# Kernel optimization log

Hardware: AMD Instinct MI355X
Metric: run time of the kernel (lower is better)

The kernel has to match this reference:

```python
import jax, jax.numpy as jnp
import numpy as np

N_HEAD, D_HEAD, D_MODEL, MAX_LEN = 16, 64, 1024, 64
T, B = 1024, 4
SCALE = 1.0 / D_HEAD ** 0.5


def setup_inputs() -> dict:
    key = jax.random.key(0)
    k1, k2, k3, k4 = jax.random.split(key, 4)
    s = 0.02
    w = jax.random.normal(k1, (T, B, D_MODEL), jnp.float32)
    Wqkv = jax.random.normal(k2, (3 * N_HEAD * D_HEAD, D_MODEL), jnp.float32) * s
    pos_emb = jax.random.normal(k3, (2 * MAX_LEN + 1, D_HEAD), jnp.float32) * s
    Wo = jax.random.normal(k4, (D_MODEL, N_HEAD * D_HEAD), jnp.float32) * s
    i = jnp.arange(T)
    # causal mask, 3D path of the original: [qlen, klen, bsz], True = masked
    attn_mask = jnp.broadcast_to((i[None, :] > i[:, None])[:, :, None], (T, T, B))
    return {"w": w, "attn_mask": attn_mask, "Wqkv": Wqkv, "pos_emb": pos_emb, "Wo": Wo}


def reference(w, attn_mask, Wqkv, pos_emb, Wo):
    qlen, bsz, _ = w.shape
    klen = qlen
    # qkv projection (no bias), chunk into q, k, v
    heads = jnp.einsum('tbd,ed->tbe', w, Wqkv)            # [T, B, 3*H*Dh]
    q, k, v = jnp.split(heads, 3, axis=-1)
    q = q.reshape(qlen, bsz, N_HEAD, D_HEAD).transpose(1, 2, 0, 3) * SCALE  # [B,H,T,Dh]
    k = k.reshape(klen, bsz, N_HEAD, D_HEAD).transpose(1, 2, 0, 3)
    v = v.reshape(klen, bsz, N_HEAD, D_HEAD).transpose(1, 2, 0, 3)
    # learnable relative position embeddings r[q_pos, k_pos, Dh]
    i = jnp.arange(klen)
    rel = jnp.clip(i[None, :] - i[:, None], -MAX_LEN, MAX_LEN) + MAX_LEN   # [T, T]
    r = pos_emb[rel]                                                       # [T, T, Dh]
    # content score + relative-position score (q already scaled)
    qk = jnp.einsum('bhqd,bhkd->bhqk', q, k)
    qr = jnp.einsum('bhqd,qkd->bhqk', q, r)
    score = qk + qr                                                        # [B,H,T,T]
    m = attn_mask.transpose(2, 0, 1)[:, None]                              # [B,1,T,T]
    score = jnp.where(m, -jnp.inf, score)
    attn = jax.nn.softmax(score, axis=-1)                                  # coverage
    # content context + position context
    ctx = jnp.einsum('bhqk,bhkd->bhqd', attn, v) + jnp.einsum('bhqk,qkd->bhqd', attn, r)
    attn_vec = ctx.transpose(0, 2, 1, 3).reshape(bsz, qlen, N_HEAD * D_HEAD)
    out = jnp.einsum('bte,de->btd', attn_vec, Wo)                          # [B,T,D]
    return jnp.swapaxes(out, 0, 1)                                         # [T,B,D]
```

## Files before the change

kernel.cpp:

```cpp
#include <hip/hip_runtime.h>
#include <hip/hip_bf16.h>
#include <math.h>

#define N_HEAD 16
#define D_HEAD 64
#define T_SEQ 1024
#define BATCH 4
#define QSCALE 0.180336879f

typedef float f32x4 __attribute__((ext_vector_type(4)));
typedef short bf16x8 __attribute__((ext_vector_type(8)));
typedef short bf16x4v __attribute__((ext_vector_type(4)));

#define AS1(p) ((const __attribute__((address_space(1))) void*)(p))
#define AS3(p) ((__attribute__((address_space(3))) void*)(p))

__device__ inline bf16x8 ld8(const __hip_bfloat16* p) {
    bf16x4v lo = *(const bf16x4v*)p;
    bf16x4v hi = *(const bf16x4v*)(p + 4);
    return __builtin_shufflevector(lo, hi, 0, 1, 2, 3, 4, 5, 6, 7);
}

__global__ __launch_bounds__(256) void cast_all(
    const float* __restrict__ s0, __hip_bfloat16* __restrict__ d0, int n0,
    const float* __restrict__ s1, __hip_bfloat16* __restrict__ d1, int n1) {
    int i = (blockIdx.x * 256 + threadIdx.x) * 8;
    const float* src;
    __hip_bfloat16* dst;
    if (i < n0) { src = s0 + i; dst = d0 + i; }
    else if ((i -= n0) < n1) { src = s1 + i; dst = d1 + i; }
    else return;
    float4 a = *(const float4*)src;
    float4 b = *(const float4*)(src + 4);
    __hip_bfloat16 t[8];
    t[0] = __float2bfloat16(a.x); t[1] = __float2bfloat16(a.y);
    t[2] = __float2bfloat16(a.z); t[3] = __float2bfloat16(a.w);
    t[4] = __float2bfloat16(b.x); t[5] = __float2bfloat16(b.y);
    t[6] = __float2bfloat16(b.z); t[7] = __float2bfloat16(b.w);
    *(uint4*)dst = *(const uint4*)t;
}

__global__ __launch_bounds__(256) void qkv_gemm_mfma(
    const __hip_bfloat16* __restrict__ A,
    const __hip_bfloat16* __restrict__ B,
    const float* __restrict__ P,
    __hip_bfloat16* __restrict__ Qb, __hip_bfloat16* __restrict__ Kb,
    __hip_bfloat16* __restrict__ Vtb) {
    constexpr int Kd = 1024;
    __shared__ __hip_bfloat16 As[128 * 32];
    __shared__ __hip_bfloat16 Bs[128 * 32];
    const int tid = threadIdx.x;
    const int w = tid >> 6, lane = tid & 63;
    const int lanelo = lane & 15, quad = lane >> 4;
    const int wm = (w >> 1) * 64, wn = (w & 1) * 64;
    const int m0 = blockIdx.y * 128, n0 = blockIdx.x * 128;

    const __hip_bfloat16* Ag = A + (size_t)(m0 + w * 16 + (lane >> 2)) * Kd + (lane & 3) * 8;
    const __hip_bfloat16* Bg = B + (size_t)(n0 + w * 16 + (lane >> 2)) * Kd + (lane & 3) * 8;
    __hip_bfloat16* AsW0 = As + w * 16 * 32;
    __hip_bfloat16* AsW1 = As + (64 + w * 16) * 32;
    __hip_bfloat16* BsW0 = Bs + w * 16 * 32;
    __hip_bfloat16* BsW1 = Bs + (64 + w * 16) * 32;

    f32x4 acc[4][4];
#pragma unroll
    for (int i = 0; i < 4; i++)
#pragma unroll
        for (int j = 0; j < 4; j++) acc[i][j] = (f32x4){0.f, 0.f, 0.f, 0.f};

    for (int k0 = 0; k0 < Kd; k0 += 32) {
        __syncthreads();
        __builtin_amdgcn_global_load_lds(AS1(Ag + k0), AS3(AsW0), 16, 0, 0);
        __builtin_amdgcn_global_load_lds(AS1(Ag + 64 * Kd + k0), AS3(AsW1), 16, 0, 0);
        __builtin_amdgcn_global_load_lds(AS1(Bg + k0), AS3(BsW0), 16, 0, 0);
        __builtin_amdgcn_global_load_lds(AS1(Bg + 64 * Kd + k0), AS3(BsW1), 16, 0, 0);
        __syncthreads();
        bf16x8 af[4], bfr[4];
#pragma unroll
        for (int i = 0; i < 4; i++)
            af[i] = *(const bf16x8*)(As + (wm + i * 16 + lanelo) * 32 + quad * 8);
#pragma unroll
        for (int j = 0; j < 4; j++)
            bfr[j] = *(const bf16x8*)(Bs + (wn + j * 16 + lanelo) * 32 + quad * 8);
#pragma unroll
        for (int i = 0; i < 4; i++)
#pragma unroll
            for (int j = 0; j < 4; j++)
                acc[i][j] = __builtin_amdgcn_mfma_f32_16x16x32_bf16(af[i], bfr[j], acc[i][j], 0, 0, 0);
    }

    const int part = n0 >> 10;
    float p0v[4] = {0.f, 0.f, 0.f, 0.f};
    if (part == 2) {
#pragma unroll
        for (int j = 0; j < 4; j++) p0v[j] = P[j * 16 + lanelo];
    }
#pragma unroll
    for (int i = 0; i < 4; i++)
#pragma unroll
        for (int j = 0; j < 4; j++)
#pragma unroll
            for (int reg = 0; reg < 4; reg++) {
                const int row = m0 + wm + i * 16 + quad * 4 + reg;
                const int col = n0 + wn + j * 16 + lanelo;
                const int t = row >> 2, b = row & 3;
                const int e = col & 1023, h = e >> 6, d = e & 63;
                const float v = acc[i][j][reg];
                if (part == 0)
                    Qb[((size_t)(b * 16 + h) * 1024 + t) * 64 + d] = __float2bfloat16(v * QSCALE);
                else if (part == 1)
                    Kb[((size_t)(b * 16 + h) * 1024 + t) * 64 + d] = __float2bfloat16(v);
                else
                    Vtb[((size_t)(b * 16 + h) * 64 + d) * 1024 + t] = __float2bfloat16(v + p0v[j]);
            }
}

__global__ __launch_bounds__(256) void out_gemm_mfma(
    const __hip_bfloat16* __restrict__ A,
    const __hip_bfloat16* __restrict__ B,
    float* __restrict__ out) {
    constexpr int Kd = 1024;
    __shared__ __hip_bfloat16 As[128 * 64];
    __shared__ __hip_bfloat16 Bs[64 * 64];
    const int tid = threadIdx.x;
    const int w = tid >> 6, lane = tid & 63;
    const int lanelo = lane & 15, quad = lane >> 4;
    const int wm = (w >> 1) * 64, wn = (w & 1) * 32;
    const int m0 = blockIdx.y * 128, n0 = blockIdx.x * 64;

    const int sr = lane >> 3;
    const int sc = ((lane & 7) ^ sr) * 8;
    const __hip_bfloat16* Ag = A + (size_t)(m0 + w * 32 + sr) * Kd + sc;
    const __hip_bfloat16* Bg = B + (size_t)(n0 + w * 16 + sr) * Kd + sc;
    __hip_bfloat16* AsW = As + w * 2048;
    __hip_bfloat16* BsW = Bs + w * 1024;

    f32x4 acc[4][2];
#pragma unroll
    for (int i = 0; i < 4; i++)
#pragma unroll
        for (int j = 0; j < 2; j++) acc[i][j] = (f32x4){0.f, 0.f, 0.f, 0.f};

    const int cswz = lanelo & 7;

    for (int k0 = 0; k0 < Kd; k0 += 64) {
        __syncthreads();
#pragma unroll
        for (int i = 0; i < 4; i++)
            __builtin_amdgcn_global_load_lds(AS1(Ag + k0 + i * 8 * Kd), AS3(AsW + i * 512), 16, 0, 0);
#pragma unroll
        for (int i = 0; i < 2; i++)
            __builtin_amdgcn_global_load_lds(AS1(Bg + k0 + i * 8 * Kd), AS3(BsW + i * 512), 16, 0, 0);
        __syncthreads();
#pragma unroll
        for (int h = 0; h < 2; h++) {
            const int c16 = (((h * 4 + quad) ^ cswz)) * 8;
            bf16x8 af[4], bfr[2];
#pragma unroll
            for (int i = 0; i < 4; i++)
                af[i] = *(const bf16x8*)(As + (size_t)(wm + i * 16 + lanelo) * 64 + c16);
#pragma unroll
            for (int j = 0; j < 2; j++)
                bfr[j] = *(const bf16x8*)(Bs + (size_t)(wn + j * 16 + lanelo) * 64 + c16);
#pragma unroll
            for (int i = 0; i < 4; i++)
#pragma unroll
                for (int j = 0; j < 2; j++)
                    acc[i][j] = __builtin_amdgcn_mfma_f32_16x16x32_bf16(af[i], bfr[j], acc[i][j], 0, 0, 0);
        }
    }

#pragma unroll
    for (int i = 0; i < 4; i++)
#pragma unroll
        for (int j = 0; j < 2; j++)
#pragma unroll
            for (int reg = 0; reg < 4; reg++) {
                const int row = m0 + wm + i * 16 + quad * 4 + reg;
                const int col = n0 + wn + j * 16 + lanelo;
                const int b = row >> 10, t = row & 1023;
                out[(size_t)(t * 4 + b) * 1024 + col] = acc[i][j][reg];
            }
}

__global__ __launch_bounds__(256) void flash_attn(
    const __hip_bfloat16* __restrict__ Qb,
    const __hip_bfloat16* __restrict__ Kb,
    const __hip_bfloat16* __restrict__ Vtb,
    const float* __restrict__ P,
    const float* __restrict__ Wo,
    __hip_bfloat16* __restrict__ Wob,
    __hip_bfloat16* __restrict__ av) {
    __shared__ __hip_bfloat16 Ks[64][72];
    __shared__ __hip_bfloat16 Vs[64][72];
    __shared__ __hip_bfloat16 Pl[4][16][68];
    __shared__ __hip_bfloat16 Pband[4][2][16][68];
    __shared__ __hip_bfloat16 QPl[4][2][16][66];

    const int px = blockIdx.x;
    const int TB = 15 - px, TS = px;
    const int bh = blockIdx.y;
    const int b = bh >> 4, h = bh & 15;
    const int tid = threadIdx.x;

    {
        const int gid = (bh * 8 + px) * 256 + tid;
        const float4 a = *(const float4*)(Wo + (size_t)gid * 8);
        const float4 c = *(const float4*)(Wo + (size_t)gid * 8 + 4);
        __hip_bfloat16 t[8];
        t[0] = __float2bfloat16(a.x); t[1] = __float2bfloat16(a.y);
        t[2] = __float2bfloat16(a.z); t[3] = __float2bfloat16(a.w);
        t[4] = __float2bfloat16(c.x); t[5] = __float2bfloat16(c.y);
        t[6] = __float2bfloat16(c.z); t[7] = __float2bfloat16(c.w);
        *(uint4*)(Wob + (size_t)gid * 8) = *(const uint4*)t;
    }

    const int w = tid >> 6, lane = tid & 63;
    const int lanelo = lane & 15, quad = lane >> 4;
    const size_t qkbase = (size_t)bh * 1024 * 64;
    const size_t vbase  = (size_t)bh * 64 * 1024;

    const int sr = tid >> 2;
    const int sc = (tid & 3) << 4;
    const __hip_bfloat16* kgb = Kb + qkbase + (size_t)sr * 64 + sc;
    const __hip_bfloat16* vgb = Vtb + vbase + (size_t)sr * 1024 + sc;

    {
        short* pb = (short*)&Pband[w][0][0][0];
        for (int i = lane; i < 2 * 16 * 68; i += 64) pb[i] = 0;
    }

    bf16x8 aqb0, aqb1, aqs0, aqs1;
    {
        const __hip_bfloat16* qrb = Qb + qkbase + (size_t)(TB * 64 + w * 16 + lanelo) * 64;
        aqb0 = *(const bf16x8*)(qrb + quad * 8);
        aqb1 = *(const bf16x8*)(qrb + 32 + quad * 8);
        const __hip_bfloat16* qrs = Qb + qkbase + (size_t)(TS * 64 + w * 16 + lanelo) * 64;
        aqs0 = *(const bf16x8*)(qrs + quad * 8);
        aqs1 = *(const bf16x8*)(qrs + 32 + quad * 8);
    }

#pragma unroll
    for (int jj = 0; jj < 5; jj++) {
        const float* prow = P + (size_t)(jj * 16 + lanelo) * 64 + quad * 8;
        float4 pa = *(const float4*)prow;
        float4 pb = *(const float4*)(prow + 4);
        float4 pc = *(const float4*)(prow + 32);
        float4 pd = *(const float4*)(prow + 36);
        __hip_bfloat16 t0[8], t1[8];
        t0[0] = __float2bfloat16(pa.x); t0[1] = __float2bfloat16(pa.y);
        t0[2] = __float2bfloat16(pa.z); t0[3] = __float2bfloat16(pa.w);
        t0[4] = __float2bfloat16(pb.x); t0[5] = __float2bfloat16(pb.y);
        t0[6] = __float2bfloat16(pb.z); t0[7] = __float2bfloat16(pb.w);
        t1[0] = __float2bfloat16(pc.x); t1[1] = __float2bfloat16(pc.y);
        t1[2] = __float2bfloat16(pc.z); t1[3] = __float2bfloat16(pc.w);
        t1[4] = __float2bfloat16(pd.x); t1[5] = __float2bfloat16(pd.y);
        t1[6] = __float2bfloat16(pd.z); t1[7] = __float2bfloat16(pd.w);
        f32x4 accB = (f32x4){0.f, 0.f, 0.f, 0.f};
        accB = __builtin_amdgcn_mfma_f32_16x16x32_bf16(aqb0, *(const bf16x8*)t0, accB, 0, 0, 0);
        accB = __builtin_amdgcn_mfma_f32_16x16x32_bf16(aqb1, *(const bf16x8*)t1, accB, 0, 0, 0);
        f32x4 accS = (f32x4){0.f, 0.f, 0.f, 0.f};
        accS = __builtin_amdgcn_mfma_f32_16x16x32_bf16(aqs0, *(const bf16x8*)t0, accS, 0, 0, 0);
        accS = __builtin_amdgcn_mfma_f32_16x16x32_bf16(aqs1, *(const bf16x8*)t1, accS, 0, 0, 0);
#pragma unroll
        for (int reg = 0; reg < 4; reg++) {
            QPl[w][0][quad * 4 + reg][jj * 16 + lanelo] = __float2bfloat16(accB[reg]);
            QPl[w][1][quad * 4 + reg][jj * 16 + lanelo] = __float2bfloat16(accS[reg]);
        }
    }
    float qp0b[4], qp0s[4];
#pragma unroll
    for (int reg = 0; reg < 4; reg++) {
        qp0b[reg] = (float)QPl[w][0][quad * 4 + reg][0];
        qp0s[reg] = (float)QPl[w][1][quad * 4 + reg][0];
    }

    f32x4 o_accB[4], o_lB, o_accS[4], o_lS;
#pragma unroll
    for (int dt = 0; dt < 4; dt++) {
        o_accB[dt] = (f32x4){0.f, 0.f, 0.f, 0.f};
        o_accS[dt] = (f32x4){0.f, 0.f, 0.f, 0.f};
    }
    o_lB = (f32x4){0.f, 0.f, 0.f, 0.f};
    o_lS = (f32x4){0.f, 0.f, 0.f, 0.f};
    const short one_bf = 0x3F80;
    const bf16x8 vones = {one_bf, one_bf, one_bf, one_bf, one_bf, one_bf, one_bf, one_bf};

    auto do_qtile = [&](int tq, int Tq, const bf16x8& a0, const bf16x8& a1,
                        const float* qp0, f32x4* o_acc, f32x4& o_l, int kt) {
        f32x4 s_acc[4];
        __builtin_amdgcn_s_setprio(1);
#pragma unroll
        for (int ct = 0; ct < 4; ct++) {
            bf16x8 b0 = *(const bf16x8*)&Ks[ct * 16 + lanelo][quad * 8];
            bf16x8 b1 = *(const bf16x8*)&Ks[ct * 16 + lanelo][32 + quad * 8];
            f32x4 acc = (f32x4){0.f, 0.f, 0.f, 0.f};
            acc = __builtin_amdgcn_mfma_f32_16x16x32_bf16(a0, b0, acc, 0, 0, 0);
            acc = __builtin_amdgcn_mfma_f32_16x16x32_bf16(a1, b1, acc, 0, 0, 0);
            s_acc[ct] = acc;
        }
        __builtin_amdgcn_s_setprio(0);
        const int q0 = Tq * 64 + w * 16;
        const int obase = q0 - kt * 64;
        if (kt < Tq - 1) {
#pragma unroll
            for (int ct = 0; ct < 4; ct++)
#pragma unroll
                for (int reg = 0; reg < 4; reg++) {
                    const float p = __builtin_exp2f(s_acc[ct][reg] + qp0[reg]);
                    Pl[w][quad * 4 + reg][ct * 16 + lanelo] = __float2bfloat16(p);
                }
        } else {
#pragma unroll
            for (int ct = 0; ct < 4; ct++)
#pragma unroll
                for (int reg = 0; reg < 4; reg++) {
                    const int rloc = quad * 4 + reg;
                    const int kl = ct * 16 + lanelo;
                    const int o = obase + rloc - kl;
                    const int idx = (o >= 64 || o < 0) ? 0 : (64 - o);
                    const float add = (float)QPl[w][tq][rloc][idx];
                    const float p = (o < 0) ? 0.f : __builtin_exp2f(s_acc[ct][reg] + add);
                    const __hip_bfloat16 pbv = __float2bfloat16(p);
                    Pl[w][rloc][kl] = pbv;
                    if (o >= 0 && o <= 63) Pband[w][tq][rloc][63 - o] = pbv;
                }
        }
        __builtin_amdgcn_s_setprio(1);
#pragma unroll
        for (int c = 0; c < 2; c++) {
            bf16x8 ap = ld8(&Pl[w][lanelo][c * 32 + quad * 8]);
#pragma unroll
            for (int dt = 0; dt < 4; dt++) {
                bf16x8 bv = *(const bf16x8*)&Vs[dt * 16 + lanelo][c * 32 + quad * 8];
                o_acc[dt] = __builtin_amdgcn_mfma_f32_16x16x32_bf16(ap, bv, o_acc[dt], 0, 0, 0);
            }
            o_l = __builtin_amdgcn_mfma_f32_16x16x32_bf16(ap, vones, o_l, 0, 0, 0);
        }
        __builtin_amdgcn_s_setprio(0);
    };

    uint4 rk0, rk1, rv0, rv1;
    rk0 = *(const uint4*)(kgb);
    rk1 = *(const uint4*)(kgb + 8);
    rv0 = *(const uint4*)(vgb);
    rv1 = *(const uint4*)(vgb + 8);

    for (int kt = 0; kt <= TB; kt++) {
        __syncthreads();
        *(uint4*)&Ks[sr][sc]     = rk0;
        *(uint4*)&Ks[sr][sc + 8] = rk1;
        *(uint4*)&Vs[sr][sc]     = rv0;
        *(uint4*)&Vs[sr][sc + 8] = rv1;
        if (kt < TB) {
            const __hip_bfloat16* kg = kgb + (size_t)(kt + 1) * 4096;
            const __hip_bfloat16* vg = vgb + (size_t)(kt + 1) * 64;
            rk0 = *(const uint4*)(kg);
            rk1 = *(const uint4*)(kg + 8);
            rv0 = *(const uint4*)(vg);
            rv1 = *(const uint4*)(vg + 8);
        }
        __syncthreads();

        do_qtile(0, TB, aqb0, aqb1, qp0b, o_accB, o_lB, kt);
        if (kt <= TS) do_qtile(1, TS, aqs0, aqs1, qp0s, o_accS, o_lS, kt);
    }

#pragma unroll
    for (int tq = 0; tq < 2; tq++) {
        f32x4* o_acc = tq == 0 ? o_accB : o_accS;
        f32x4& o_l   = tq == 0 ? o_lB : o_lS;
        const int q0 = (tq == 0 ? TB : TS) * 64 + w * 16;
#pragma unroll
        for (int c = 0; c < 2; c++) {
            bf16x8 ab = ld8(&Pband[w][tq][lanelo][c * 32 + quad * 8]);
#pragma unroll
            for (int dt = 0; dt < 4; dt++) {
                const int d = dt * 16 + lanelo;
                const float p0 = P[d];
                __hip_bfloat16 tb[8];
#pragma unroll
                for (int jj = 0; jj < 8; jj++) {
                    const int kk = c * 32 + quad * 8 + jj;
                    tb[jj] = __float2bfloat16(P[(kk + 1) * 64 + d] - p0);
                }
                o_acc[dt] = __builtin_amdgcn_mfma_f32_16x16x32_bf16(ab, *(const bf16x8*)tb, o_acc[dt], 0, 0, 0);
            }
        }
        float rinv[4];
#pragma unroll
        for (int reg = 0; reg < 4; reg++) rinv[reg] = 1.0f / o_l[reg];
#pragma unroll
        for (int dt = 0; dt < 4; dt++) {
            const int cdim = dt * 16 + lanelo;
#pragma unroll
            for (int reg = 0; reg < 4; reg++) {
                const int q = q0 + quad * 4 + reg;
                av[((size_t)(b * 1024 + q)) * 1024 + h * 64 + cdim] =
                    __float2bfloat16(o_acc[dt][reg] * rinv[reg]);
            }
        }
    }
}

extern "C" void kernel_launch(void* const* d_in, const int* in_sizes, int n_in,
                              void* d_out, int out_size, void* d_ws, size_t ws_size,
                              hipStream_t stream) {
    const float* w       = (const float*)d_in[0];
    const float* Wqkv    = (const float*)d_in[2];
    const float* pos_emb = (const float*)d_in[3];
    const float* Wo      = (const float*)d_in[4];
    float* out = (float*)d_out;

    const size_t SZ = (size_t)BATCH * N_HEAD * T_SEQ * D_HEAD;
    __hip_bfloat16* wb     = (__hip_bfloat16*)d_ws;
    __hip_bfloat16* Wqkvb  = wb + SZ;
    __hip_bfloat16* Wob    = Wqkvb + 3 * 1024 * 1024;
    __hip_bfloat16* Qb     = Wob + 1024 * 1024;
    __hip_bfloat16* Kb     = Qb + SZ;
    __hip_bfloat16* Vtb    = Kb + SZ;
    __hip_bfloat16* AVb    = Vtb + SZ;

    const int n_w = 4096 * 1024, n_wqkv = 3072 * 1024;
    const int n_tot = n_w + n_wqkv;
    cast_all<<<n_tot / 2048, 256, 0, stream>>>(w, wb, n_w, Wqkv, Wqkvb, n_wqkv);

    qkv_gemm_mfma<<<dim3(3072 / 128, 4096 / 128), 256, 0, stream>>>(wb, Wqkvb, pos_emb, Qb, Kb, Vtb);
    flash_attn<<<dim3(8, 64), 256, 0, stream>>>(Qb, Kb, Vtb, pos_emb, Wo, Wob, AVb);
    out_gemm_mfma<<<dim3(1024 / 64, 4096 / 128), 256, 0, stream>>>(AVb, Wob, out);
}
```

Baseline: 187.1 us.

## Fuse kernel pairs with software grid barriers to cut launch count

Merges the cast and QKV GEMM into one persistent-style launch, and flash attention plus the output GEMM into another. Each pair is separated by an atomic-counter grid barrier, with the counters kept in the first words of the output buffer and zeroed by a memset. This removes two kernel launch gaps and tail effects. It relies on all 768 (or 512) blocks being co-resident, otherwise it deadlocks. The output buffer doubles as semaphore storage, which is safe only because the final GEMM overwrites those words after the barrier.

```diff
diff --git a/kernel.cpp b/kernel.cpp
--- a/kernel.cpp
+++ b/kernel.cpp
@@ -21,46 +21,63 @@
     return __builtin_shufflevector(lo, hi, 0, 1, 2, 3, 4, 5, 6, 7);
 }
 
-__global__ __launch_bounds__(256) void cast_all(
-    const float* __restrict__ s0, __hip_bfloat16* __restrict__ d0, int n0,
-    const float* __restrict__ s1, __hip_bfloat16* __restrict__ d1, int n1) {
-    int i = (blockIdx.x * 256 + threadIdx.x) * 8;
-    const float* src;
-    __hip_bfloat16* dst;
-    if (i < n0) { src = s0 + i; dst = d0 + i; }
-    else if ((i -= n0) < n1) { src = s1 + i; dst = d1 + i; }
-    else return;
-    float4 a = *(const float4*)src;
-    float4 b = *(const float4*)(src + 4);
-    __hip_bfloat16 t[8];
-    t[0] = __float2bfloat16(a.x); t[1] = __float2bfloat16(a.y);
-    t[2] = __float2bfloat16(a.z); t[3] = __float2bfloat16(a.w);
-    t[4] = __float2bfloat16(b.x); t[5] = __float2bfloat16(b.y);
-    t[6] = __float2bfloat16(b.z); t[7] = __float2bfloat16(b.w);
-    *(uint4*)dst = *(const uint4*)t;
+__device__ inline void grid_barrier(unsigned int* sem, unsigned int target) {
+    __threadfence();
+    __syncthreads();
+    if (threadIdx.x == 0) {
+        __hip_atomic_fetch_add(sem, 1u, __ATOMIC_RELEASE, __HIP_MEMORY_SCOPE_AGENT);
+        while (__hip_atomic_load(sem, __ATOMIC_ACQUIRE, __HIP_MEMORY_SCOPE_AGENT) < target)
+            __builtin_amdgcn_s_sleep(2);
+    }
+    __syncthreads();
+    __threadfence();
 }
 
-__global__ __launch_bounds__(256) void qkv_gemm_mfma(
-    const __hip_bfloat16* __restrict__ A,
-    const __hip_bfloat16* __restrict__ B,
+__global__ __launch_bounds__(256) void cast_qkv_fused(
+    const float* __restrict__ w,
+    const float* __restrict__ Wqkv,
     const float* __restrict__ P,
+    __hip_bfloat16* __restrict__ wb, __hip_bfloat16* __restrict__ Wqkvb,
     __hip_bfloat16* __restrict__ Qb, __hip_bfloat16* __restrict__ Kb,
-    __hip_bfloat16* __restrict__ Vtb) {
+    __hip_bfloat16* __restrict__ Vtb,
+    unsigned int* sem) {
     constexpr int Kd = 1024;
+    constexpr int n_w = 4096 * 1024;
+    constexpr int n_tot = n_w + 3072 * 1024;
     __shared__ __hip_bfloat16 As[128 * 32];
     __shared__ __hip_bfloat16 Bs[128 * 32];
     const int tid = threadIdx.x;
-    const int w = tid >> 6, lane = tid & 63;
+
+    for (int i = ((int)blockIdx.x * 256 + tid) * 8; i < n_tot; i += 768 * 256 * 8) {
+        const float* src;
+        __hip_bfloat16* dst;
+        if (i < n_w) { src = w + i; dst = wb + i; }
+        else         { src = Wqkv + (i - n_w); dst = Wqkvb + (i - n_w); }
+        float4 a = *(const float4*)src;
+        float4 c = *(const float4*)(src + 4);
+        __hip_bfloat16 t[8];
+        t[0] = __float2bfloat16(a.x); t[1] = __float2bfloat16(a.y);
+        t[2] = __float2bfloat16(a.z); t[3] = __float2bfloat16(a.w);
+        t[4] = __float2bfloat16(c.x); t[5] = __float2bfloat16(c.y);
+        t[6] = __float2bfloat16(c.z); t[7] = __float2bfloat16(c.w);
+        *(uint4*)dst = *(const uint4*)t;
+    }
+
+    grid_barrier(sem, 768);
+
+    const int bid = blockIdx.x;
+    const int bx = bid % 24, by = bid / 24;
+    const int m0 = by * 128, n0 = bx * 128;
+    const int wv = tid >> 6, lane = tid & 63;
     const int lanelo = lane & 15, quad = lane >> 4;
-    const int wm = (w >> 1) * 64, wn = (w & 1) * 64;
-    const int m0 = blockIdx.y * 128, n0 = blockIdx.x * 128;
-
-    const __hip_bfloat16* Ag = A + (size_t)(m0 + w * 16 + (lane >> 2)) * Kd + (lane & 3) * 8;
-    const __hip_bfloat16* Bg = B + (size_t)(n0 + w * 16 + (lane >> 2)) * Kd + (lane & 3) * 8;
-    __hip_bfloat16* AsW0 = As + w * 16 * 32;
-    __hip_bfloat16* AsW1 = As + (64 + w * 16) * 32;
-    __hip_bfloat16* BsW0 = Bs + w * 16 * 32;
-    __hip_bfloat16* BsW1 = Bs + (64 + w * 16) * 32;
+    const int wm = (wv >> 1) * 64, wn = (wv & 1) * 64;
+
+    const __hip_bfloat16* Ag = wb + (size_t)(m0 + wv * 16 + (lane >> 2)) * Kd + (lane & 3) * 8;
+    const __hip_bfloat16* Bg = Wqkvb + (size_t)(n0 + wv * 16 + (lane >> 2)) * Kd + (lane & 3) * 8;
+    __hip_bfloat16* AsW0 = As + wv * 16 * 32;
+    __hip_bfloat16* AsW1 = As + (64 + wv * 16) * 32;
+    __hip_bfloat16* BsW0 = Bs + wv * 16 * 32;
+    __hip_bfloat16* BsW1 = Bs + (64 + wv * 16) * 32;
 
     f32x4 acc[4][4];
 #pragma unroll
@@ -115,96 +132,34 @@
             }
 }
 
-__global__ __launch_bounds__(256) void out_gemm_mfma(
-    const __hip_bfloat16* __restrict__ A,
-    const __hip_bfloat16* __restrict__ B,
-    float* __restrict__ out) {
-    constexpr int Kd = 1024;
-    __shared__ __hip_bfloat16 As[128 * 64];
-    __shared__ __hip_bfloat16 Bs[64 * 64];
-    const int tid = threadIdx.x;
-    const int w = tid >> 6, lane = tid & 63;
-    const int lanelo = lane & 15, quad = lane >> 4;
-    const int wm = (w >> 1) * 64, wn = (w & 1) * 32;
-    const int m0 = blockIdx.y * 128, n0 = blockIdx.x * 64;
-
-    const int sr = lane >> 3;
-    const int sc = ((lane & 7) ^ sr) * 8;
-    const __hip_bfloat16* Ag = A + (size_t)(m0 + w * 32 + sr) * Kd + sc;
-    const __hip_bfloat16* Bg = B + (size_t)(n0 + w * 16 + sr) * Kd + sc;
-    __hip_bfloat16* AsW = As + w * 2048;
-    __hip_bfloat16* BsW = Bs + w * 1024;
-
-    f32x4 acc[4][2];
-#pragma unroll
-    for (int i = 0; i < 4; i++)
-#pragma unroll
-        for (int j = 0; j < 2; j++) acc[i][j] = (f32x4){0.f, 0.f, 0.f, 0.f};
-
-    const int cswz = lanelo & 7;
-
-    for (int k0 = 0; k0 < Kd; k0 += 64) {
-        __syncthreads();
-#pragma unroll
-        for (int i = 0; i < 4; i++)
-            __builtin_amdgcn_global_load_lds(AS1(Ag + k0 + i * 8 * Kd), AS3(AsW + i * 512), 16, 0, 0);
-#pragma unroll
-        for (int i = 0; i < 2; i++)
-            __builtin_amdgcn_global_load_lds(AS1(Bg + k0 + i * 8 * Kd), AS3(BsW + i * 512), 16, 0, 0);
-        __syncthreads();
-#pragma unroll
-        for (int h = 0; h < 2; h++) {
-            const int c16 = (((h * 4 + quad) ^ cswz)) * 8;
-            bf16x8 af[4], bfr[2];
-#pragma unroll
-            for (int i = 0; i < 4; i++)
-                af[i] = *(const bf16x8*)(As + (size_t)(wm + i * 16 + lanelo) * 64 + c16);
-#pragma unroll
-            for (int j = 0; j < 2; j++)
-                bfr[j] = *(const bf16x8*)(Bs + (size_t)(wn + j * 16 + lanelo) * 64 + c16);
-#pragma unroll
-            for (int i = 0; i < 4; i++)
-#pragma unroll
-                for (int j = 0; j < 2; j++)
-                    acc[i][j] = __builtin_amdgcn_mfma_f32_16x16x32_bf16(af[i], bfr[j], acc[i][j], 0, 0, 0);
-        }
-    }
-
-#pragma unroll
-    for (int i = 0; i < 4; i++)
-#pragma unroll
-        for (int j = 0; j < 2; j++)
-#pragma unroll
-            for (int reg = 0; reg < 4; reg++) {
-                const int row = m0 + wm + i * 16 + quad * 4 + reg;
-                const int col = n0 + wn + j * 16 + lanelo;
-                const int b = row >> 10, t = row & 1023;
-                out[(size_t)(t * 4 + b) * 1024 + col] = acc[i][j][reg];
-            }
-}
-
-__global__ __launch_bounds__(256) void flash_attn(
+__global__ __launch_bounds__(256) void flash_out_fused(
     const __hip_bfloat16* __restrict__ Qb,
     const __hip_bfloat16* __restrict__ Kb,
     const __hip_bfloat16* __restrict__ Vtb,
     const float* __restrict__ P,
     const float* __restrict__ Wo,
     __hip_bfloat16* __restrict__ Wob,
-    __hip_bfloat16* __restrict__ av) {
-    __shared__ __hip_bfloat16 Ks[64][72];
-    __shared__ __hip_bfloat16 Vs[64][72];
-    __shared__ __hip_bfloat16 Pl[4][16][68];
-    __shared__ __hip_bfloat16 Pband[4][2][16][68];
-    __shared__ __hip_bfloat16 QPl[4][2][16][66];
-
-    const int px = blockIdx.x;
+    __hip_bfloat16* __restrict__ av,
+    float* __restrict__ out,
+    unsigned int* sem) {
+    __shared__ __align__(16) char smem[61440];
+    auto Ks    = reinterpret_cast<__hip_bfloat16(*)[72]>(smem);
+    auto Vs    = reinterpret_cast<__hip_bfloat16(*)[72]>(smem + 9216);
+    auto Pl    = reinterpret_cast<__hip_bfloat16(*)[16][68]>(smem + 18432);
+    auto Pband = reinterpret_cast<__hip_bfloat16(*)[2][16][68]>(smem + 27136);
+    auto QPl   = reinterpret_cast<__hip_bfloat16(*)[2][16][66]>(smem + 44544);
+
+    const int bid = blockIdx.x;
+    const int tid = threadIdx.x;
+
+    {
+    const int px = bid & 7;
     const int TB = 15 - px, TS = px;
-    const int bh = blockIdx.y;
+    const int bh = bid >> 3;
     const int b = bh >> 4, h = bh & 15;
-    const int tid = threadIdx.x;
 
     {
-        const int gid = (bh * 8 + px) * 256 + tid;
+        const int gid = bid * 256 + tid;
         const float4 a = *(const float4*)(Wo + (size_t)gid * 8);
         const float4 c = *(const float4*)(Wo + (size_t)gid * 8 + 4);
         __hip_bfloat16 t[8];
@@ -401,6 +356,75 @@
             }
         }
     }
+    }
+
+    grid_barrier(sem, 512);
+
+    {
+    constexpr int Kd = 1024;
+    __hip_bfloat16* As = reinterpret_cast<__hip_bfloat16*>(smem);
+    __hip_bfloat16* Bs = reinterpret_cast<__hip_bfloat16*>(smem + 16384);
+
+    const int w = tid >> 6, lane = tid & 63;
+    const int lanelo = lane & 15, quad = lane >> 4;
+    const int wm = (w >> 1) * 64, wn = (w & 1) * 32;
+    const int bx = bid & 15, by = bid >> 4;
+    const int m0 = by * 128, n0 = bx * 64;
+
+    const int sr = lane >> 3;
+    const int sc = ((lane & 7) ^ sr) * 8;
+    const __hip_bfloat16* Ag = av + (size_t)(m0 + w * 32 + sr) * Kd + sc;
+    const __hip_bfloat16* Bg = Wob + (size_t)(n0 + w * 16 + sr) * Kd + sc;
+    __hip_bfloat16* AsW = As + w * 2048;
+    __hip_bfloat16* BsW = Bs + w * 1024;
+
+    f32x4 acc[4][2];
+#pragma unroll
+    for (int i = 0; i < 4; i++)
+#pragma unroll
+        for (int j = 0; j < 2; j++) acc[i][j] = (f32x4){0.f, 0.f, 0.f, 0.f};
+
+    const int cswz = lanelo & 7;
+
+    for (int k0 = 0; k0 < Kd; k0 += 64) {
+        __syncthreads();
+#pragma unroll
+        for (int i = 0; i < 4; i++)
+            __builtin_amdgcn_global_load_lds(AS1(Ag + k0 + i * 8 * Kd), AS3(AsW + i * 512), 16, 0, 0);
+#pragma unroll
+        for (int i = 0; i < 2; i++)
+            __builtin_amdgcn_global_load_lds(AS1(Bg + k0 + i * 8 * Kd), AS3(BsW + i * 512), 16, 0, 0);
+        __syncthreads();
+#pragma unroll
+        for (int h = 0; h < 2; h++) {
+            const int c16 = (((h * 4 + quad) ^ cswz)) * 8;
+            bf16x8 af[4], bfr[2];
+#pragma unroll
+            for (int i = 0; i < 4; i++)
+                af[i] = *(const bf16x8*)(As + (size_t)(wm + i * 16 + lanelo) * 64 + c16);
+#pragma unroll
+            for (int j = 0; j < 2; j++)
+                bfr[j] = *(const bf16x8*)(Bs + (size_t)(wn + j * 16 + lanelo) * 64 + c16);
+#pragma unroll
+            for (int i = 0; i < 4; i++)
+#pragma unroll
+                for (int j = 0; j < 2; j++)
+                    acc[i][j] = __builtin_amdgcn_mfma_f32_16x16x32_bf16(af[i], bfr[j], acc[i][j], 0, 0, 0);
+        }
+    }
+
+#pragma unroll
+    for (int i = 0; i < 4; i++)
+#pragma unroll
+        for (int j = 0; j < 2; j++)
+#pragma unroll
+            for (int reg = 0; reg < 4; reg++) {
+                const int row = m0 + wm + i * 16 + quad * 4 + reg;
+                const int col = n0 + wn + j * 16 + lanelo;
+                const int b = row >> 10, t = row & 1023;
+                out[(size_t)(t * 4 + b) * 1024 + col] = acc[i][j][reg];
+            }
+    }
 }
 
 extern "C" void kernel_launch(void* const* d_in, const int* in_sizes, int n_in,
@@ -421,11 +445,11 @@
     __hip_bfloat16* Vtb    = Kb + SZ;
     __hip_bfloat16* AVb    = Vtb + SZ;
 
-    const int n_w = 4096 * 1024, n_wqkv = 3072 * 1024;
-    const int n_tot = n_w + n_wqkv;
-    cast_all<<<n_tot / 2048, 256, 0, stream>>>(w, wb, n_w, Wqkv, Wqkvb, n_wqkv);
-
-    qkv_gemm_mfma<<<dim3(3072 / 128, 4096 / 128), 256, 0, stream>>>(wb, Wqkvb, pos_emb, Qb, Kb, Vtb);
-    flash_attn<<<dim3(8, 64), 256, 0, stream>>>(Qb, Kb, Vtb, pos_emb, Wo, Wob, AVb);
-    out_gemm_mfma<<<dim3(1024 / 64, 4096 / 128), 256, 0, stream>>>(AVb, Wob, out);
+    unsigned int* sem = (unsigned int*)out;
+    hipMemsetAsync(out, 0, 8, stream);
+
+    cast_qkv_fused<<<dim3(768), 256, 0, stream>>>(w, Wqkv, pos_emb, wb, Wqkvb,
+                                                  Qb, Kb, Vtb, sem);
+    flash_out_fused<<<dim3(512), 256, 0, stream>>>(Qb, Kb, Vtb, pos_emb, Wo, Wob,
+                                                   AVb, out, sem + 1);
 }
```

Result: slower. 499.5 us (+167.0%).
